# Optimization experiments

Hardware: AMD Instinct MI355X
Metric: run time of the kernel (lower is better)

The kernel has to match this reference:

```python
import jax, jax.numpy as jnp
import numpy as np

N = 100000      # nodes
E = 1600000     # edges (avg degree 16)
G = 1000        # graphs in batch
F_IN = 128      # num_features
C = 10          # num_classes
EPS = 1e-5


def setup_inputs() -> dict:
    key = jax.random.key(0)
    ks = jax.random.split(key, 12)
    w = lambda k, shape: jax.random.normal(k, shape, jnp.float32) * 0.05
    return {
        'x': jax.random.normal(ks[0], (N, F_IN), jnp.float32),
        'edge_index': jax.random.randint(ks[1], (2, E), 0, N, jnp.int32),
        'edge_weights': jax.random.randint(ks[2], (E,), 0, 2, jnp.int32),
        'batch': jnp.sort(jax.random.randint(ks[3], (N,), 0, G, jnp.int32)),
        'num_graphs': G,
        # initial MLP: Linear(128,32)+BN+ReLU, Linear(32,32)+BN+ReLU
        'W1': w(ks[4], (F_IN, 32)), 'b1': jnp.zeros(32), 'g1': jnp.ones(32), 'bt1': jnp.zeros(32),
        'W2': w(ks[5], (32, 32)), 'b2': jnp.zeros(32), 'g2': jnp.ones(32), 'bt2': jnp.zeros(32),
        'Wl0': w(ks[6], (32, C)), 'bl0': jnp.zeros(C),   # initial_linear
        'Wg1': w(ks[7], (32, 64)), 'bg1': jnp.zeros(64),  # GCNConv 1
        'Wl1': w(ks[8], (64, C)), 'bl1': jnp.zeros(C),
        'Wg2': w(ks[9], (64, 64)), 'bg2': jnp.zeros(64),  # GCNConv 2
        'Wl2': w(ks[10], (64, C)), 'bl2': jnp.zeros(C),
    }


def _bn(h, gamma, beta):
    # BatchNorm1d in training mode: biased batch statistics over nodes
    mu = h.mean(0)
    var = ((h - mu) ** 2).mean(0)
    return gamma * (h - mu) * jax.lax.rsqrt(var + EPS) + beta


def _gcn(h_in, row, col, w, W, b):
    # PyG GCNConv with self-loops: D^{-1/2}(A+I)D^{-1/2} X W + b,
    # edges with mask weight 0 contribute nothing (incl. to degree).
    n = h_in.shape[0]
    h = h_in @ W
    deg = jax.ops.segment_sum(w, col, num_segments=n) + 1.0  # +1 self-loop
    dinv = jax.lax.rsqrt(deg)
    norm = w * dinv[row] * dinv[col]                  # [E]
    agg = jax.ops.segment_sum(h[row] * norm[:, None], col, num_segments=n)
    agg = agg + h * (dinv * dinv)[:, None]            # self-loop term
    return agg + b


def _pool_max(h, batch, num_graphs):
    # torch_scatter scatter_max readout; empty segments -> 0
    p = jax.ops.segment_max(h, batch, num_segments=num_graphs)
    return jnp.where(jnp.isfinite(p), p, 0.0)


def reference(x, edge_index, edge_weights, batch, num_graphs,
              W1, b1, g1, bt1, W2, b2, g2, bt2, Wl0, bl0,
              Wg1, bg1, Wl1, bl1, Wg2, bg2, Wl2, bl2):
    row, col = edge_index[0], edge_index[1]
    w = (edge_weights == 1).astype(x.dtype)  # boolean edge mask as 0/1 weight
    # initial MLP (dropout treated as identity for deterministic reference)
    h = jax.nn.relu(_bn(x @ W1 + b1, g1, bt1))
    h = jax.nn.relu(_bn(h @ W2 + b2, g2, bt2))
    out = _pool_max(h @ Wl0 + bl0, batch, num_graphs)
    # layer 1
    h = _gcn(h, row, col, w, Wg1, bg1)
    out = out + _pool_max(h, batch, num_graphs) @ Wl1 + bl1
    # layer 2
    h = _gcn(h, row, col, w, Wg2, bg2)
    out = out + _pool_max(h, batch, num_graphs) @ Wl2 + bl2
    return out
```

## Files before the change

kernel.cpp:

```cpp
#include <hip/hip_runtime.h>

#define NN 100000
#define EE 1600000
#define GG 1000
#define BN_EPS 1e-5f
#define NB1 391
#define NTB 782

__device__ __forceinline__ unsigned encf(float f){
  unsigned u = __float_as_uint(f);
  return (u & 0x80000000u) ? ~u : (u | 0x80000000u);
}
__device__ __forceinline__ float dec0(unsigned e){
  unsigned u = (e & 0x80000000u) ? (e & 0x7fffffffu) : ~e;
  float f = __uint_as_float(u);
  return isfinite(f) ? f : 0.0f;
}
__device__ __forceinline__ unsigned short f2bf(float f){
  unsigned u = __float_as_uint(f);
  u += 0x7FFFu + ((u >> 16) & 1u);
  return (unsigned short)(u >> 16);
}
__device__ __forceinline__ float bf2f(unsigned short s){
  return __uint_as_float(((unsigned)s) << 16);
}

#define STEP4(AX, WV) \
  acc[0][0]=fmaf(a0.AX,WV.x,acc[0][0]); acc[0][1]=fmaf(a0.AX,WV.y,acc[0][1]); \
  acc[0][2]=fmaf(a0.AX,WV.z,acc[0][2]); acc[0][3]=fmaf(a0.AX,WV.w,acc[0][3]); \
  acc[1][0]=fmaf(a1.AX,WV.x,acc[1][0]); acc[1][1]=fmaf(a1.AX,WV.y,acc[1][1]); \
  acc[1][2]=fmaf(a1.AX,WV.z,acc[1][2]); acc[1][3]=fmaf(a1.AX,WV.w,acc[1][3]); \
  acc[2][0]=fmaf(a2.AX,WV.x,acc[2][0]); acc[2][1]=fmaf(a2.AX,WV.y,acc[2][1]); \
  acc[2][2]=fmaf(a2.AX,WV.z,acc[2][2]); acc[2][3]=fmaf(a2.AX,WV.w,acc[2][3]); \
  acc[3][0]=fmaf(a3.AX,WV.x,acc[3][0]); acc[3][1]=fmaf(a3.AX,WV.y,acc[3][1]); \
  acc[3][2]=fmaf(a3.AX,WV.z,acc[3][2]); acc[3][3]=fmaf(a3.AX,WV.w,acc[3][3]);

__global__ void k_count(const int* __restrict__ ei, const int* __restrict__ ew,
                        int* __restrict__ cnt){
  int e = blockIdx.x*256 + threadIdx.x;
  if (e < EE && ew[e] == 1) atomicAdd(&cnt[ei[EE + e]], 1);
}

__global__ __launch_bounds__(256) void k_alloc(const int* __restrict__ cnt,
    int* __restrict__ ctr, float* __restrict__ dinv,
    int* __restrict__ rowstart, int* __restrict__ fill){
  __shared__ int sm[256];
  __shared__ int base;
  const int i = blockIdx.x*256 + threadIdx.x;
  const int v = (i < NN) ? cnt[i] : 0;
  sm[threadIdx.x] = v;
  __syncthreads();
  for (int off = 1; off < 256; off <<= 1){
    int t = (threadIdx.x >= off) ? sm[threadIdx.x - off] : 0;
    __syncthreads();
    sm[threadIdx.x] += t;
    __syncthreads();
  }
  if (threadIdx.x == 255) base = atomicAdd(ctr, sm[255]);
  __syncthreads();
  if (i < NN){
    int rs = base + sm[threadIdx.x] - v;
    rowstart[i] = rs; fill[i] = rs;
    dinv[i] = rsqrtf((float)v + 1.0f);
  }
}

__global__ void k_scatter(const int* __restrict__ ei, const int* __restrict__ ew,
                          int* __restrict__ fill, int* __restrict__ csr){
  int e = blockIdx.x*256 + threadIdx.x;
  if (e < EE && ew[e] == 1){
    int c = ei[EE + e];
    int pos = atomicAdd(&fill[c], 1);
    csr[pos] = ei[e];
  }
}

__global__ __launch_bounds__(256) void k_gemm1(const float* __restrict__ x,
    const float* __restrict__ W1, const float* __restrict__ b1,
    unsigned short* __restrict__ Y1b, float* __restrict__ stats){
  __shared__ float xs[128*68];
  __shared__ float Ws[64*32];
  __shared__ float red[64];
  const int tid = threadIdx.x;
  if (tid < 64) red[tid] = 0.f;
  const int rg = tid >> 3, cg = tid & 7;
  const float4 bv = ((const float4*)b1)[cg];
  float acc[4][4];
  #pragma unroll
  for (int i = 0; i < 4; i++){ acc[i][0]=bv.x; acc[i][1]=bv.y; acc[i][2]=bv.z; acc[i][3]=bv.w; }
  const long rowbase = (long)blockIdx.x*128;
  #pragma unroll
  for (int half = 0; half < 2; half++){
    __syncthreads();
    for (int j = tid; j < 512; j += 256){
      int kk = j >> 3, cc = j & 7;
      ((float4*)Ws)[j] = ((const float4*)W1)[(size_t)(half*64 + kk)*8 + cc];
    }
    for (int j = tid; j < 2048; j += 256){
      int rr = j >> 4, kk = j & 15;
      long gr = rowbase + rr;
      float4 v = (gr < NN) ? ((const float4*)(x + gr*128 + half*64))[kk]
                           : float4{0.f,0.f,0.f,0.f};
      *(float4*)&xs[rr*68 + kk*4] = v;
    }
    __syncthreads();
    #pragma unroll 4
    for (int k = 0; k < 64; k += 4){
      const float4 a0 = *(const float4*)&xs[(rg     )*68 + k];
      const float4 a1 = *(const float4*)&xs[(rg + 32)*68 + k];
      const float4 a2 = *(const float4*)&xs[(rg + 64)*68 + k];
      const float4 a3 = *(const float4*)&xs[(rg + 96)*68 + k];
      const float4 w0 = *(const float4*)&Ws[(k+0)*32 + cg*4];
      const float4 w1 = *(const float4*)&Ws[(k+1)*32 + cg*4];
      const float4 w2 = *(const float4*)&Ws[(k+2)*32 + cg*4];
      const float4 w3 = *(const float4*)&Ws[(k+3)*32 + cg*4];
      STEP4(x, w0) STEP4(y, w1) STEP4(z, w2) STEP4(w, w3)
    }
  }
  float s[4] = {0,0,0,0}, q[4] = {0,0,0,0};
  #pragma unroll
  for (int i = 0; i < 4; i++){
    const long r = rowbase + rg + 32*i;
    if (r < NN){
      ushort4 o; o.x=f2bf(acc[i][0]); o.y=f2bf(acc[i][1]); o.z=f2bf(acc[i][2]); o.w=f2bf(acc[i][3]);
      ((ushort4*)Y1b)[r*8 + cg] = o;
      #pragma unroll
      for (int j = 0; j < 4; j++){ s[j] += acc[i][j]; q[j] += acc[i][j]*acc[i][j]; }
    }
  }
  __syncthreads();
  #pragma unroll
  for (int j = 0; j < 4; j++){
    atomicAdd(&red[cg*4+j], s[j]);
    atomicAdd(&red[32+cg*4+j], q[j]);
  }
  __syncthreads();
  if (tid < 64) atomicAdd(&stats[tid], red[tid]);
}

__global__ __launch_bounds__(256) void k_mlp2(const unsigned short* __restrict__ Y1b,
    const float* __restrict__ W2, const float* __restrict__ b2,
    const float* __restrict__ g1, const float* __restrict__ bt1,
    float* __restrict__ stats, unsigned short* __restrict__ Y2b){
  __shared__ float ht[128*36];
  __shared__ float Ws[32*32];
  __shared__ float red[64];
  __shared__ float scs[32], shs[32];
  const int tid = threadIdx.x;
  ((float4*)Ws)[tid] = ((const float4*)W2)[tid];
  if (tid < 64) red[tid] = 0.f;
  if (tid < 32){
    float mean = stats[tid] * (1.0f/NN);
    float var  = stats[32 + tid] * (1.0f/NN) - mean*mean;
    float sH = g1[tid] * rsqrtf(fmaxf(var, 0.0f) + BN_EPS);
    scs[tid] = sH; shs[tid] = bt1[tid] - mean*sH;
  }
  __syncthreads();
  const long rowbase = (long)blockIdx.x*128;
  for (int j = tid; j < 1024; j += 256){
    int rr = j >> 3, kk = j & 7;
    long gr = rowbase + rr;
    ushort4 u = (gr < NN) ? ((const ushort4*)Y1b)[gr*8 + kk] : ushort4{0,0,0,0};
    float4 v;
    v.x = fmaxf(fmaf(bf2f(u.x), scs[kk*4+0], shs[kk*4+0]), 0.f);
    v.y = fmaxf(fmaf(bf2f(u.y), scs[kk*4+1], shs[kk*4+1]), 0.f);
    v.z = fmaxf(fmaf(bf2f(u.z), scs[kk*4+2], shs[kk*4+2]), 0.f);
    v.w = fmaxf(fmaf(bf2f(u.w), scs[kk*4+3], shs[kk*4+3]), 0.f);
    *(float4*)&ht[rr*36 + kk*4] = v;
  }
  __syncthreads();
  const int rg = tid >> 3, cg = tid & 7;
  const float4 bv = ((const float4*)b2)[cg];
  float acc[4][4];
  #pragma unroll
  for (int i = 0; i < 4; i++){ acc[i][0]=bv.x; acc[i][1]=bv.y; acc[i][2]=bv.z; acc[i][3]=bv.w; }
  #pragma unroll
  for (int k = 0; k < 32; k += 4){
    const float4 a0 = *(const float4*)&ht[(rg     )*36 + k];
    const float4 a1 = *(const float4*)&ht[(rg + 32)*36 + k];
    const float4 a2 = *(const float4*)&ht[(rg + 64)*36 + k];
    const float4 a3 = *(const float4*)&ht[(rg + 96)*36 + k];
    const float4 w0 = *(const float4*)&Ws[(k+0)*32 + cg*4];
    const float4 w1 = *(const float4*)&Ws[(k+1)*32 + cg*4];
    const float4 w2 = *(const float4*)&Ws[(k+2)*32 + cg*4];
    const float4 w3 = *(const float4*)&Ws[(k+3)*32 + cg*4];
    STEP4(x, w0) STEP4(y, w1) STEP4(z, w2) STEP4(w, w3)
  }
  float s[4] = {0,0,0,0}, q[4] = {0,0,0,0};
  #pragma unroll
  for (int i = 0; i < 4; i++){
    const long r = rowbase + rg + 32*i;
    if (r < NN){
      ushort4 o; o.x=f2bf(acc[i][0]); o.y=f2bf(acc[i][1]); o.z=f2bf(acc[i][2]); o.w=f2bf(acc[i][3]);
      ((ushort4*)Y2b)[r*8 + cg] = o;
      #pragma unroll
      for (int j = 0; j < 4; j++){ s[j] += acc[i][j]; q[j] += acc[i][j]*acc[i][j]; }
    }
  }
  __syncthreads();
  #pragma unroll
  for (int j = 0; j < 4; j++){
    atomicAdd(&red[cg*4+j], s[j]);
    atomicAdd(&red[32+cg*4+j], q[j]);
  }
  __syncthreads();
  if (tid < 64) atomicAdd(&stats[128 + tid], red[tid]);
}

__global__ __launch_bounds__(256) void k_layer0(const unsigned short* __restrict__ Y2b,
    const float* __restrict__ stats, const float* __restrict__ g2,
    const float* __restrict__ bt2, const float* __restrict__ Wg1,
    const float* __restrict__ Wl0, const float* __restrict__ bl0,
    const float* __restrict__ dinv, const int* __restrict__ batch,
    unsigned short* __restrict__ Hs1, unsigned* __restrict__ Pool0){
  __shared__ float hs[32*36];
  __shared__ float Wg[32*64];
  __shared__ float Wl[320];
  __shared__ float bl[10];
  __shared__ float scs[32], shs[32];
  const int tid = threadIdx.x;
  ((float4*)Wg)[tid]       = ((const float4*)Wg1)[tid];
  ((float4*)Wg)[tid + 256] = ((const float4*)Wg1)[tid + 256];
  for (int j = tid; j < 320; j += 256) Wl[j] = Wl0[j];
  if (tid < 10)  bl[tid] = bl0[tid];
  if (tid < 32){
    float mean = stats[128 + tid] * (1.0f/NN);
    float var  = stats[160 + tid] * (1.0f/NN) - mean*mean;
    float s = g2[tid] * rsqrtf(fmaxf(var, 0.0f) + BN_EPS);
    scs[tid] = s; shs[tid] = bt2[tid] - mean*s;
  }
  __syncthreads();
  {
    const int rr = tid >> 3, kk = tid & 7;
    const float4 sc = *(const float4*)&scs[kk*4];
    const float4 sh = *(const float4*)&shs[kk*4];
    ushort4 u = ((const ushort4*)Y2b)[(size_t)blockIdx.x*256 + tid];
    float4 v;
    v.x = fmaxf(fmaf(bf2f(u.x), sc.x, sh.x), 0.f);
    v.y = fmaxf(fmaf(bf2f(u.y), sc.y, sh.y), 0.f);
    v.z = fmaxf(fmaf(bf2f(u.z), sc.z, sh.z), 0.f);
    v.w = fmaxf(fmaf(bf2f(u.w), sc.w, sh.w), 0.f);
    *(float4*)&hs[rr*36 + kk*4] = v;
  }
  __syncthreads();
  const int w = tid >> 6, f = tid & 63;
  for (int i = 0; i < 8; i++){
    const int r = w*8 + i;
    const int row = blockIdx.x*32 + r;
    const float* hr = &hs[r*36];
    float acc = 0.f;
    #pragma unroll
    for (int k = 0; k < 32; k++) acc += hr[k]*Wg[k*64 + f];
    Hs1[(size_t)row*64 + f] = f2bf(acc * dinv[row]);
    if (f < 10){
      float p = bl[f];
      #pragma unroll
      for (int k = 0; k < 32; k++) p += hr[k]*Wl[k*10 + f];
      atomicMax(&Pool0[batch[row]*10 + f], encf(p));
    }
  }
}

__device__ __forceinline__ float gather_sum(const unsigned short* __restrict__ Hs,
    const int* __restrict__ csr, int s, int e, int f){
  float acc = 0.f;
  int j = s;
  for (; j + 7 < e; j += 8){
    const int r0 = csr[j],   r1 = csr[j+1], r2 = csr[j+2], r3 = csr[j+3];
    const int r4 = csr[j+4], r5 = csr[j+5], r6 = csr[j+6], r7 = csr[j+7];
    float t0 = bf2f(Hs[(size_t)r0*64 + f]);
    float t1 = bf2f(Hs[(size_t)r1*64 + f]);
    float t2 = bf2f(Hs[(size_t)r2*64 + f]);
    float t3 = bf2f(Hs[(size_t)r3*64 + f]);
    float t4 = bf2f(Hs[(size_t)r4*64 + f]);
    float t5 = bf2f(Hs[(size_t)r5*64 + f]);
    float t6 = bf2f(Hs[(size_t)r6*64 + f]);
    float t7 = bf2f(Hs[(size_t)r7*64 + f]);
    acc += ((t0 + t1) + (t2 + t3)) + ((t4 + t5) + (t6 + t7));
  }
  for (; j + 3 < e; j += 4){
    const int r0 = csr[j], r1 = csr[j+1], r2 = csr[j+2], r3 = csr[j+3];
    float t0 = bf2f(Hs[(size_t)r0*64 + f]);
    float t1 = bf2f(Hs[(size_t)r1*64 + f]);
    float t2 = bf2f(Hs[(size_t)r2*64 + f]);
    float t3 = bf2f(Hs[(size_t)r3*64 + f]);
    acc += (t0 + t1) + (t2 + t3);
  }
  for (; j < e; j++) acc += bf2f(Hs[(size_t)csr[j]*64 + f]);
  return acc;
}

__device__ __forceinline__ void pool_epilogue(float h, int w, int f, int c,
    const int* __restrict__ batch, unsigned* __restrict__ Pool,
    float (*sm)[64], int* sb){
  sm[w][f] = h;
  if (f == 0) sb[w] = batch[c];
  __syncthreads();
  if (w == 0){
    const int b0 = sb[0], b1 = sb[1], b2 = sb[2], b3 = sb[3];
    if (b0 == b3){
      float m = fmaxf(fmaxf(sm[0][f], sm[1][f]), fmaxf(sm[2][f], sm[3][f]));
      atomicMax(&Pool[b0*64 + f], encf(m));
    } else {
      atomicMax(&Pool[b0*64 + f], encf(sm[0][f]));
      atomicMax(&Pool[b1*64 + f], encf(sm[1][f]));
      atomicMax(&Pool[b2*64 + f], encf(sm[2][f]));
      atomicMax(&Pool[b3*64 + f], encf(sm[3][f]));
    }
  }
}

__global__ __launch_bounds__(256) void k_agg1(const unsigned short* __restrict__ Hs,
    const float* __restrict__ dinv, const int* __restrict__ rowstart,
    const int* __restrict__ cnt, const int* __restrict__ csr,
    const float* __restrict__ bias, const int* __restrict__ batch,
    unsigned short* __restrict__ H2b, unsigned* __restrict__ Pool){
  __shared__ float sm[4][64];
  __shared__ int sb[4];
  const int w = threadIdx.x >> 6, f = threadIdx.x & 63;
  const int c = blockIdx.x*4 + w;
  const int s = rowstart[c], e = s + cnt[c];
  float acc = gather_sum(Hs, csr, s, e, f);
  const float dc = dinv[c];
  const float h = fmaf(acc + bf2f(Hs[(size_t)c*64 + f]), dc, bias[f]);
  H2b[(size_t)c*64 + f] = f2bf(h);
  pool_epilogue(h, w, f, c, batch, Pool, sm, sb);
}

__global__ __launch_bounds__(256) void k_agg2(const unsigned short* __restrict__ Hs,
    const float* __restrict__ dinv, const int* __restrict__ rowstart,
    const int* __restrict__ cnt, const int* __restrict__ csr,
    const float* __restrict__ bias, const int* __restrict__ batch,
    unsigned* __restrict__ Pool){
  __shared__ float sm[4][64];
  __shared__ int sb[4];
  const int w = threadIdx.x >> 6, f = threadIdx.x & 63;
  const int c = blockIdx.x*4 + w;
  const int s = rowstart[c], e = s + cnt[c];
  float acc = gather_sum(Hs, csr, s, e, f);
  const float dc = dinv[c];
  const float h = fmaf(acc + bf2f(Hs[(size_t)c*64 + f]), dc, bias[f]);
  pool_epilogue(h, w, f, c, batch, Pool, sm, sb);
}

__global__ __launch_bounds__(256) void k_layer1(const unsigned short* __restrict__ H2b,
    const float* __restrict__ Wg2, const float* __restrict__ dinv,
    unsigned short* __restrict__ Hs2){
  __shared__ float as[32*68];
  __shared__ float Wg[64*64];
  const int tid = threadIdx.x;
  #pragma unroll
  for (int j = 0; j < 4; j++) ((float4*)Wg)[tid + j*256] = ((const float4*)Wg2)[tid + j*256];
  {
    const int rr = tid >> 3, kk = tid & 7;
    ushort4 v0 = ((const ushort4*)H2b)[(size_t)blockIdx.x*512 + tid*2];
    ushort4 v1 = ((const ushort4*)H2b)[(size_t)blockIdx.x*512 + tid*2 + 1];
    float* dst = &as[rr*68 + kk*8];
    dst[0]=bf2f(v0.x); dst[1]=bf2f(v0.y); dst[2]=bf2f(v0.z); dst[3]=bf2f(v0.w);
    dst[4]=bf2f(v1.x); dst[5]=bf2f(v1.y); dst[6]=bf2f(v1.z); dst[7]=bf2f(v1.w);
  }
  __syncthreads();
  const int w = tid >> 6, f = tid & 63;
  for (int i = 0; i < 8; i++){
    const int r = w*8 + i;
    const int row = blockIdx.x*32 + r;
    const float* ar = &as[r*68];
    float acc = 0.f;
    #pragma unroll
    for (int k = 0; k < 64; k++) acc += ar[k]*Wg[k*64 + f];
    Hs2[(size_t)row*64 + f] = f2bf(acc * dinv[row]);
  }
}

__global__ __launch_bounds__(256) void k_final(const unsigned* __restrict__ P0,
    const unsigned* __restrict__ P1, const unsigned* __restrict__ P2,
    const float* __restrict__ Wl1, const float* __restrict__ bl1,
    const float* __restrict__ Wl2, const float* __restrict__ bl2,
    float* __restrict__ out){
  const int t = blockIdx.x*256 + threadIdx.x;
  const int g = t >> 4, c = t & 15;
  if (g >= GG || c >= 10) return;
  float acc = dec0(P0[g*10 + c]) + bl1[c] + bl2[c];
  for (int f = 0; f < 64; f++){
    acc += dec0(P1[g*64 + f]) * Wl1[f*10 + c];
    acc += dec0(P2[g*64 + f]) * Wl2[f*10 + c];
  }
  out[g*10 + c] = acc;
}

extern "C" void kernel_launch(void* const* d_in, const int* in_sizes, int n_in,
                              void* d_out, int out_size, void* d_ws, size_t ws_size,
                              hipStream_t stream){
  const float* x   = (const float*)d_in[0];
  const int*   ei  = (const int*)d_in[1];
  const int*   ew  = (const int*)d_in[2];
  const int*   bat = (const int*)d_in[3];
  const float* W1  = (const float*)d_in[5],  *b1  = (const float*)d_in[6];
  const float* g1  = (const float*)d_in[7],  *bt1 = (const float*)d_in[8];
  const float* W2  = (const float*)d_in[9],  *b2  = (const float*)d_in[10];
  const float* g2  = (const float*)d_in[11], *bt2 = (const float*)d_in[12];
  const float* Wl0 = (const float*)d_in[13], *bl0 = (const float*)d_in[14];
  const float* Wg1 = (const float*)d_in[15], *bg1 = (const float*)d_in[16];
  const float* Wl1 = (const float*)d_in[17], *bl1 = (const float*)d_in[18];
  const float* Wg2 = (const float*)d_in[19], *bg2 = (const float*)d_in[20];
  const float* Wl2 = (const float*)d_in[21], *bl2 = (const float*)d_in[22];

  float* ws = (float*)d_ws;
  const size_t oCnt   = 0;
  const size_t oCtr   = NN;
  const size_t oStats = NN + 8;
  const size_t oP0    = oStats + 256;
  const size_t oP1    = oP0 + (size_t)GG*10;
  const size_t oP2    = oP1 + (size_t)GG*64;
  const size_t oZEnd  = oP2 + (size_t)GG*64;
  const size_t oDinv  = oZEnd;
  const size_t oRS    = oDinv + NN;
  const size_t oFill  = oRS + NN;
  const size_t oCsr   = oFill + NN;
  const size_t oR1    = oCsr + EE;
  const size_t oR2    = oR1 + (size_t)NN*16;
  const size_t oR3    = oR2 + (size_t)NN*16;
  const size_t oR4    = oR3 + (size_t)NN*32;

  int*   cnt   = (int*)(ws + oCnt);
  int*   ctr   = (int*)(ws + oCtr);
  float* stats = ws + oStats;
  unsigned* P0 = (unsigned*)(ws + oP0);
  unsigned* P1 = (unsigned*)(ws + oP1);
  unsigned* P2 = (unsigned*)(ws + oP2);
  float* dinv  = ws + oDinv;
  int*   rs    = (int*)(ws + oRS);
  int*   fill  = (int*)(ws + oFill);
  int*   csr   = (int*)(ws + oCsr);
  unsigned short* Y1b = (unsigned short*)(ws + oR1);
  unsigned short* Y2b = (unsigned short*)(ws + oR2);
  unsigned short* Hs1 = (unsigned short*)(ws + oR3);
  unsigned short* Hs2 = (unsigned short*)(ws + oR3);
  unsigned short* H2b = (unsigned short*)(ws + oR4);

  (void)hipMemsetAsync(d_ws, 0, oZEnd*sizeof(float), stream);

  k_count  <<<EE/256, 256, 0, stream>>>(ei, ew, cnt);
  k_alloc  <<<NB1, 256, 0, stream>>>(cnt, ctr, dinv, rs, fill);
  k_scatter<<<EE/256, 256, 0, stream>>>(ei, ew, fill, csr);

  k_gemm1<<<NTB, 256, 0, stream>>>(x, W1, b1, Y1b, stats);
  k_mlp2 <<<NTB, 256, 0, stream>>>(Y1b, W2, b2, g1, bt1, stats, Y2b);
  k_layer0<<<3125, 256, 0, stream>>>(Y2b, stats, g2, bt2, Wg1, Wl0, bl0, dinv, bat, Hs1, P0);
  k_agg1 <<<NN/4, 256, 0, stream>>>(Hs1, dinv, rs, cnt, csr, bg1, bat, H2b, P1);
  k_layer1<<<3125, 256, 0, stream>>>(H2b, Wg2, dinv, Hs2);
  k_agg2 <<<NN/4, 256, 0, stream>>>(Hs2, dinv, rs, cnt, csr, bg2, bat, P2);
  k_final<<<(GG*16 + 255)/256, 256, 0, stream>>>(P0, P1, P2, Wl1, bl1, Wl2, bl2, (float*)d_out);
}
```

Baseline: 342.1 us.

## Co-schedule CSR build with MLP stages in fused launches; stage x as bf16

The three CSR-building kernels (degree count, prefix-sum allocation, edge scatter) are merged into the three dense MLP/layer0 kernels as extra blocks. Block indices are interleaved so each fused launch runs independent graph-preprocessing work alongside dense compute. This removes three launches and lets atomic-heavy edge work overlap with the GEMMs. The first GEMM also stores its x tile in shared memory as bf16 instead of fp32, which halves the LDS footprint and store traffic but rounds the input features before the multiply and adds conversion instructions.

```diff
diff --git a/kernel.cpp b/kernel.cpp
--- a/kernel.cpp
+++ b/kernel.cpp
@@ -35,50 +35,21 @@
   acc[3][0]=fmaf(a3.AX,WV.x,acc[3][0]); acc[3][1]=fmaf(a3.AX,WV.y,acc[3][1]); \
   acc[3][2]=fmaf(a3.AX,WV.z,acc[3][2]); acc[3][3]=fmaf(a3.AX,WV.w,acc[3][3]);
 
-__global__ void k_count(const int* __restrict__ ei, const int* __restrict__ ew,
-                        int* __restrict__ cnt){
-  int e = blockIdx.x*256 + threadIdx.x;
-  if (e < EE && ew[e] == 1) atomicAdd(&cnt[ei[EE + e]], 1);
-}
-
-__global__ __launch_bounds__(256) void k_alloc(const int* __restrict__ cnt,
-    int* __restrict__ ctr, float* __restrict__ dinv,
-    int* __restrict__ rowstart, int* __restrict__ fill){
-  __shared__ int sm[256];
-  __shared__ int base;
-  const int i = blockIdx.x*256 + threadIdx.x;
-  const int v = (i < NN) ? cnt[i] : 0;
-  sm[threadIdx.x] = v;
-  __syncthreads();
-  for (int off = 1; off < 256; off <<= 1){
-    int t = (threadIdx.x >= off) ? sm[threadIdx.x - off] : 0;
-    __syncthreads();
-    sm[threadIdx.x] += t;
-    __syncthreads();
-  }
-  if (threadIdx.x == 255) base = atomicAdd(ctr, sm[255]);
-  __syncthreads();
-  if (i < NN){
-    int rs = base + sm[threadIdx.x] - v;
-    rowstart[i] = rs; fill[i] = rs;
-    dinv[i] = rsqrtf((float)v + 1.0f);
-  }
-}
-
-__global__ void k_scatter(const int* __restrict__ ei, const int* __restrict__ ew,
-                          int* __restrict__ fill, int* __restrict__ csr){
-  int e = blockIdx.x*256 + threadIdx.x;
-  if (e < EE && ew[e] == 1){
-    int c = ei[EE + e];
-    int pos = atomicAdd(&fill[c], 1);
-    csr[pos] = ei[e];
-  }
-}
-
-__global__ __launch_bounds__(256) void k_gemm1(const float* __restrict__ x,
-    const float* __restrict__ W1, const float* __restrict__ b1,
-    unsigned short* __restrict__ Y1b, float* __restrict__ stats){
-  __shared__ float xs[128*68];
+__global__ __launch_bounds__(256) void k_d1(
+    const int* __restrict__ ei, const int* __restrict__ ew, int* __restrict__ cnt,
+    const float* __restrict__ x, const float* __restrict__ W1,
+    const float* __restrict__ b1, unsigned short* __restrict__ Y1b,
+    float* __restrict__ stats){
+  const int bi = blockIdx.x;
+  if ((bi & 7) != 7){
+    const int ce = bi - (bi >> 3);
+    const int e = ce*256 + threadIdx.x;
+    if (e < EE && ew[e] == 1) atomicAdd(&cnt[ei[EE + e]], 1);
+    return;
+  }
+  const int tile = bi >> 3;
+  if (tile >= NTB) return;
+  __shared__ unsigned short xs[128*72];
   __shared__ float Ws[64*32];
   __shared__ float red[64];
   const int tid = threadIdx.x;
@@ -88,7 +59,7 @@
   float acc[4][4];
   #pragma unroll
   for (int i = 0; i < 4; i++){ acc[i][0]=bv.x; acc[i][1]=bv.y; acc[i][2]=bv.z; acc[i][3]=bv.w; }
-  const long rowbase = (long)blockIdx.x*128;
+  const long rowbase = (long)tile*128;
   #pragma unroll
   for (int half = 0; half < 2; half++){
     __syncthreads();
@@ -101,15 +72,21 @@
       long gr = rowbase + rr;
       float4 v = (gr < NN) ? ((const float4*)(x + gr*128 + half*64))[kk]
                            : float4{0.f,0.f,0.f,0.f};
-      *(float4*)&xs[rr*68 + kk*4] = v;
+      ushort4 u; u.x=f2bf(v.x); u.y=f2bf(v.y); u.z=f2bf(v.z); u.w=f2bf(v.w);
+      *(ushort4*)&xs[rr*72 + kk*4] = u;
     }
     __syncthreads();
     #pragma unroll 4
     for (int k = 0; k < 64; k += 4){
-      const float4 a0 = *(const float4*)&xs[(rg     )*68 + k];
-      const float4 a1 = *(const float4*)&xs[(rg + 32)*68 + k];
-      const float4 a2 = *(const float4*)&xs[(rg + 64)*68 + k];
-      const float4 a3 = *(const float4*)&xs[(rg + 96)*68 + k];
+      const ushort4 u0 = *(const ushort4*)&xs[(rg     )*72 + k];
+      const ushort4 u1 = *(const ushort4*)&xs[(rg + 32)*72 + k];
+      const ushort4 u2 = *(const ushort4*)&xs[(rg + 64)*72 + k];
+      const ushort4 u3 = *(const ushort4*)&xs[(rg + 96)*72 + k];
+      float4 a0, a1, a2, a3;
+      a0.x=bf2f(u0.x); a0.y=bf2f(u0.y); a0.z=bf2f(u0.z); a0.w=bf2f(u0.w);
+      a1.x=bf2f(u1.x); a1.y=bf2f(u1.y); a1.z=bf2f(u1.z); a1.w=bf2f(u1.w);
+      a2.x=bf2f(u2.x); a2.y=bf2f(u2.y); a2.z=bf2f(u2.z); a2.w=bf2f(u2.w);
+      a3.x=bf2f(u3.x); a3.y=bf2f(u3.y); a3.z=bf2f(u3.z); a3.w=bf2f(u3.w);
       const float4 w0 = *(const float4*)&Ws[(k+0)*32 + cg*4];
       const float4 w1 = *(const float4*)&Ws[(k+1)*32 + cg*4];
       const float4 w2 = *(const float4*)&Ws[(k+2)*32 + cg*4];
@@ -138,10 +115,39 @@
   if (tid < 64) atomicAdd(&stats[tid], red[tid]);
 }
 
-__global__ __launch_bounds__(256) void k_mlp2(const unsigned short* __restrict__ Y1b,
-    const float* __restrict__ W2, const float* __restrict__ b2,
-    const float* __restrict__ g1, const float* __restrict__ bt1,
-    float* __restrict__ stats, unsigned short* __restrict__ Y2b){
+__global__ __launch_bounds__(256) void k_d2(
+    const int* __restrict__ cnt, int* __restrict__ ctr, float* __restrict__ dinv,
+    int* __restrict__ rowstart, int* __restrict__ fill,
+    const unsigned short* __restrict__ Y1b, const float* __restrict__ W2,
+    const float* __restrict__ b2, const float* __restrict__ g1,
+    const float* __restrict__ bt1, float* __restrict__ stats,
+    unsigned short* __restrict__ Y2b){
+  const int bi = blockIdx.x;
+  if (bi % 3 == 0){
+    const int ab = bi/3;
+    if (ab >= NB1) return;
+    __shared__ int sm[256];
+    __shared__ int base;
+    const int i = ab*256 + threadIdx.x;
+    const int v = (i < NN) ? cnt[i] : 0;
+    sm[threadIdx.x] = v;
+    __syncthreads();
+    for (int off = 1; off < 256; off <<= 1){
+      int t = (threadIdx.x >= off) ? sm[threadIdx.x - off] : 0;
+      __syncthreads();
+      sm[threadIdx.x] += t;
+      __syncthreads();
+    }
+    if (threadIdx.x == 255) base = atomicAdd(ctr, sm[255]);
+    __syncthreads();
+    if (i < NN){
+      int rs = base + sm[threadIdx.x] - v;
+      rowstart[i] = rs; fill[i] = rs;
+      dinv[i] = rsqrtf((float)v + 1.0f);
+    }
+    return;
+  }
+  const int tile = bi - bi/3 - 1;
   __shared__ float ht[128*36];
   __shared__ float Ws[32*32];
   __shared__ float red[64];
@@ -156,7 +162,7 @@
     scs[tid] = sH; shs[tid] = bt1[tid] - mean*sH;
   }
   __syncthreads();
-  const long rowbase = (long)blockIdx.x*128;
+  const long rowbase = (long)tile*128;
   for (int j = tid; j < 1024; j += 256){
     int rr = j >> 3, kk = j & 7;
     long gr = rowbase + rr;
@@ -207,12 +213,27 @@
   if (tid < 64) atomicAdd(&stats[128 + tid], red[tid]);
 }
 
-__global__ __launch_bounds__(256) void k_layer0(const unsigned short* __restrict__ Y2b,
-    const float* __restrict__ stats, const float* __restrict__ g2,
-    const float* __restrict__ bt2, const float* __restrict__ Wg1,
-    const float* __restrict__ Wl0, const float* __restrict__ bl0,
-    const float* __restrict__ dinv, const int* __restrict__ batch,
-    unsigned short* __restrict__ Hs1, unsigned* __restrict__ Pool0){
+__global__ __launch_bounds__(256) void k_d3(
+    const int* __restrict__ ei, const int* __restrict__ ew,
+    int* __restrict__ fill, int* __restrict__ csr,
+    const unsigned short* __restrict__ Y2b, const float* __restrict__ stats,
+    const float* __restrict__ g2, const float* __restrict__ bt2,
+    const float* __restrict__ Wg1, const float* __restrict__ Wl0,
+    const float* __restrict__ bl0, const float* __restrict__ dinv,
+    const int* __restrict__ batch, unsigned short* __restrict__ Hs1,
+    unsigned* __restrict__ Pool0){
+  const int bi = blockIdx.x;
+  if (bi % 3 != 2){
+    const int se = bi - bi/3;
+    const int e = se*256 + threadIdx.x;
+    if (e < EE && ew[e] == 1){
+      int c = ei[EE + e];
+      int pos = atomicAdd(&fill[c], 1);
+      csr[pos] = ei[e];
+    }
+    return;
+  }
+  const int blk = bi/3;
   __shared__ float hs[32*36];
   __shared__ float Wg[32*64];
   __shared__ float Wl[320];
@@ -234,7 +255,7 @@
     const int rr = tid >> 3, kk = tid & 7;
     const float4 sc = *(const float4*)&scs[kk*4];
     const float4 sh = *(const float4*)&shs[kk*4];
-    ushort4 u = ((const ushort4*)Y2b)[(size_t)blockIdx.x*256 + tid];
+    ushort4 u = ((const ushort4*)Y2b)[(size_t)blk*256 + tid];
     float4 v;
     v.x = fmaxf(fmaf(bf2f(u.x), sc.x, sh.x), 0.f);
     v.y = fmaxf(fmaf(bf2f(u.y), sc.y, sh.y), 0.f);
@@ -246,7 +267,7 @@
   const int w = tid >> 6, f = tid & 63;
   for (int i = 0; i < 8; i++){
     const int r = w*8 + i;
-    const int row = blockIdx.x*32 + r;
+    const int row = blk*32 + r;
     const float* hr = &hs[r*36];
     float acc = 0.f;
     #pragma unroll
@@ -440,13 +461,9 @@
 
   (void)hipMemsetAsync(d_ws, 0, oZEnd*sizeof(float), stream);
 
-  k_count  <<<EE/256, 256, 0, stream>>>(ei, ew, cnt);
-  k_alloc  <<<NB1, 256, 0, stream>>>(cnt, ctr, dinv, rs, fill);
-  k_scatter<<<EE/256, 256, 0, stream>>>(ei, ew, fill, csr);
-
-  k_gemm1<<<NTB, 256, 0, stream>>>(x, W1, b1, Y1b, stats);
-  k_mlp2 <<<NTB, 256, 0, stream>>>(Y1b, W2, b2, g1, bt1, stats, Y2b);
-  k_layer0<<<3125, 256, 0, stream>>>(Y2b, stats, g2, bt2, Wg1, Wl0, bl0, dinv, bat, Hs1, P0);
+  k_d1<<<7144, 256, 0, stream>>>(ei, ew, cnt, x, W1, b1, Y1b, stats);
+  k_d2<<<1173, 256, 0, stream>>>(cnt, ctr, dinv, rs, fill, Y1b, W2, b2, g1, bt1, stats, Y2b);
+  k_d3<<<9375, 256, 0, stream>>>(ei, ew, fill, csr, Y2b, stats, g2, bt2, Wg1, Wl0, bl0, dinv, bat, Hs1, P0);
   k_agg1 <<<NN/4, 256, 0, stream>>>(Hs1, dinv, rs, cnt, csr, bg1, bat, H2b, P1);
   k_layer1<<<3125, 256, 0, stream>>>(H2b, Wg2, dinv, Hs2);
   k_agg2 <<<NN/4, 256, 0, stream>>>(Hs2, dinv, rs, cnt, csr, bg2, bat, P2);
```

After: 434.0 us. +26.9%, slower.
